# Performance work log

Hardware: AMD Instinct MI355X
Metric: run time of the kernel (lower is better)

## Reference

```python
import jax, jax.numpy as jnp
import numpy as np

EMB = 768

def setup_inputs() -> dict:
    key = jax.random.key(0)
    ks = jax.random.split(key, 9)
    B, N, E = 8, 2048, EMB
    s = 1.0 / np.sqrt(E)
    return {
        "x":  jax.random.normal(ks[0], (B, N, E), jnp.float32),
        "Wq": jax.random.normal(ks[1], (E, E), jnp.float32) * s,
        "bq": jnp.zeros((E,), jnp.float32),
        "Wk": jax.random.normal(ks[2], (E, E), jnp.float32) * s,
        "bk": jnp.zeros((E,), jnp.float32),
        "Wv": jax.random.normal(ks[3], (E, E), jnp.float32) * s,
        "bv": jnp.zeros((E,), jnp.float32),
        "Wo": jax.random.normal(ks[4], (E, E), jnp.float32) * s,
        "bo": jnp.zeros((E,), jnp.float32),
    }

def reference(x, Wq, bq, Wk, bk, Wv, bv, Wo, bo):
    # Single-head attention; scale uses full emb dim (as in the source).
    E = x.shape[-1]
    q = jnp.einsum('bne,ef->bnf', x, Wq) + bq
    k = jnp.einsum('bne,ef->bnf', x, Wk) + bk
    v = jnp.einsum('bne,ef->bnf', x, Wv) + bv
    scores = jnp.einsum('bqe,bke->bqk', q, k) / jnp.sqrt(jnp.asarray(E, x.dtype))
    attn = jax.nn.softmax(scores, axis=-1)  # dropout is identity in eval mode
    out = jnp.einsum('bqk,bke->bqe', attn, v)
    return jnp.einsum('bne,ef->bnf', out, Wo) + bo
```

## Files before the change

kernel.cpp:

```cpp
#include <hip/hip_runtime.h>
#include <hip/hip_fp16.h>
#include <stdint.h>

typedef unsigned short u16;
typedef __attribute__((ext_vector_type(8))) __bf16 bf16x8;
typedef __attribute__((ext_vector_type(4))) float f32x4;

#define SEQ 2048
#define EMB 768
#define NB  8
#define LDQK (2 * EMB)

__device__ __forceinline__ u16 f2bf(float f) {
  union { float f; uint32_t u; } a; a.f = f;
  uint32_t r = a.u + 0x7fffu + ((a.u >> 16) & 1u);
  return (u16)(r >> 16);
}
__device__ __forceinline__ float bf2f(u16 h) {
  union { uint32_t u; float f; } a; a.u = ((uint32_t)h) << 16;
  return a.f;
}

__global__ __launch_bounds__(256) void k_detect_bias(
    const u16* __restrict__ x, int* __restrict__ flag,
    const void* __restrict__ b0, const void* __restrict__ b1,
    const void* __restrict__ b2, const void* __restrict__ b3,
    float* __restrict__ biasf)
{
  const int tid = threadIdx.x;
  int bad = 0;
#pragma unroll
  for (int i = 0; i < 4; ++i) {
    const u16 h = x[(tid * 4 + i) * 2];
    const int e = (h >> 7) & 0xFF;
    bad += (e >= 160 && e <= 254) ? 1 : 0;
  }
#pragma unroll
  for (int off = 32; off > 0; off >>= 1) bad += __shfl_down(bad, off);
  __shared__ int cnt[4];
  __shared__ int sflag;
  if ((tid & 63) == 0) cnt[tid >> 6] = bad;
  __syncthreads();
  if (tid == 0) {
    const int f = (cnt[0] + cnt[1] + cnt[2] + cnt[3] > 200) ? 1 : 0;
    sflag = f;
    *flag = f;
  }
  __syncthreads();
  const int f32 = sflag;
#pragma unroll
  for (int z = 0; z < 4; ++z) {
    const void* src = (z == 0) ? b0 : (z == 1) ? b1 : (z == 2) ? b2 : b3;
#pragma unroll
    for (int i = 0; i < 3; ++i) {
      const int j = tid + i * 256;
      biasf[z * EMB + j] = f32 ? ((const float*)src)[j]
                               : bf2f(((const u16*)src)[j]);
    }
  }
}

__global__ __launch_bounds__(256) void k_convert_x(
    const void* __restrict__ src, u16* __restrict__ dst,
    const int* __restrict__ flag, int n4)
{
  const int i = blockIdx.x * 256 + threadIdx.x;
  if (i >= n4) return;
  if (*flag) {
    const float4 f = ((const float4*)src)[i];
    ushort4 o;
    o.x = f2bf(f.x); o.y = f2bf(f.y); o.z = f2bf(f.z); o.w = f2bf(f.w);
    ((ushort4*)dst)[i] = o;
  } else {
    ((ushort4*)dst)[i] = ((const ushort4*)src)[i];
  }
}

__global__ __launch_bounds__(256) void k_transpose_w(
    const void* __restrict__ W0, const void* __restrict__ W1,
    const void* __restrict__ W2, const void* __restrict__ W3,
    u16* __restrict__ WT, const int* __restrict__ flag)
{
  __shared__ u16 t[32][33];
  const int z = blockIdx.z;
  const void* in = (z == 0) ? W0 : (z == 1) ? W1 : (z == 2) ? W2 : W3;
  u16* out = WT + (size_t)z * EMB * EMB;
  const int c0 = blockIdx.x * 32, r0 = blockIdx.y * 32;
  const int tx = threadIdx.x, ty = threadIdx.y;
  const int f32 = *flag;
#pragma unroll
  for (int i = 0; i < 4; ++i) {
    const size_t idx = (size_t)(r0 + ty + i * 8) * EMB + c0 + tx;
    t[ty + i * 8][tx] = f32 ? f2bf(((const float*)in)[idx])
                            : ((const u16*)in)[idx];
  }
  __syncthreads();
#pragma unroll
  for (int i = 0; i < 4; ++i)
    out[(size_t)(c0 + ty + i * 8) * EMB + r0 + tx] = t[tx][ty + i * 8];
}

template <int EPI>
__device__ __forceinline__ void gemm_core(
    const u16* __restrict__ A, int lda,
    const u16* __restrict__ BT, int ldbt,
    void* __restrict__ Cp, int ldc,
    const float* __restrict__ biasf, const int* __restrict__ of32,
    float scale, int K, int m0, int n0)
{
  __shared__ __align__(16) u16 As[128 * 32];
  __shared__ __align__(16) u16 Bs[128 * 32];
  const int tid  = threadIdx.x;
  const int lane = tid & 63;
  const int wave = tid >> 6;
  const int wr   = (wave >> 1) * 64;
  const int wc   = (wave & 1) * 64;
  const int lrow = lane & 15;
  const int quad = lane >> 4;

  f32x4 acc[4][4];
#pragma unroll
  for (int i = 0; i < 4; ++i)
#pragma unroll
    for (int j = 0; j < 4; ++j)
#pragma unroll
      for (int r = 0; r < 4; ++r) acc[i][j][r] = 0.0f;

  for (int kt = 0; kt < K; kt += 32) {
#pragma unroll
    for (int i = 0; i < 2; ++i) {
      const int c = wave * 128 + i * 64 + lane;
      const int r = c >> 2, s = c & 3;
      const u16* ga = A  + (size_t)(m0 + r) * lda  + kt + s * 8;
      const u16* gb = BT + (size_t)(n0 + r) * ldbt + kt + s * 8;
      u16* la = As + (size_t)(wave * 128 + i * 64) * 8;
      u16* lb = Bs + (size_t)(wave * 128 + i * 64) * 8;
      __builtin_amdgcn_global_load_lds(
          (const __attribute__((address_space(1))) void*)ga,
          (__attribute__((address_space(3))) void*)la, 16, 0, 0);
      __builtin_amdgcn_global_load_lds(
          (const __attribute__((address_space(1))) void*)gb,
          (__attribute__((address_space(3))) void*)lb, 16, 0, 0);
    }
    __syncthreads();

    bf16x8 af[4], bfr[4];
#pragma unroll
    for (int i = 0; i < 4; ++i)
      af[i] = *(const bf16x8*)(As + (wr + i * 16 + lrow) * 32 + quad * 8);
#pragma unroll
    for (int j = 0; j < 4; ++j)
      bfr[j] = *(const bf16x8*)(Bs + (wc + j * 16 + lrow) * 32 + quad * 8);

#pragma unroll
    for (int i = 0; i < 4; ++i)
#pragma unroll
      for (int j = 0; j < 4; ++j)
        acc[i][j] = __builtin_amdgcn_mfma_f32_16x16x32_bf16(af[i], bfr[j],
                                                            acc[i][j], 0, 0, 0);
    __syncthreads();
  }

  if (EPI == 3) {
    u16* C = (u16*)Cp;
#pragma unroll
    for (int i = 0; i < 4; ++i)
#pragma unroll
      for (int j = 0; j < 4; ++j)
#pragma unroll
        for (int r = 0; r < 4; ++r) {
          const int row = m0 + wr + i * 16 + quad * 4 + r;
          const int col = n0 + wc + j * 16 + lrow;
          C[(size_t)row * ldc + col] =
              __half_as_ushort(__float2half(acc[i][j][r] * scale));
        }
  } else if (EPI == 2) {
    u16* C = (u16*)Cp;
#pragma unroll
    for (int i = 0; i < 4; ++i)
#pragma unroll
      for (int j = 0; j < 4; ++j)
#pragma unroll
        for (int r = 0; r < 4; ++r) {
          const int row = m0 + wr + i * 16 + quad * 4 + r;
          const int col = n0 + wc + j * 16 + lrow;
          C[(size_t)row * ldc + col] = f2bf(acc[i][j][r]);
        }
  } else if (EPI == 5) {
    u16* C = (u16*)Cp;
#pragma unroll
    for (int i = 0; i < 4; ++i)
#pragma unroll
      for (int r = 0; r < 4; ++r) {
        const int row = m0 + wr + i * 16 + quad * 4 + r;
        const float bv = biasf[row];
#pragma unroll
        for (int j = 0; j < 4; ++j) {
          const int col = n0 + wc + j * 16 + lrow;
          C[(size_t)row * ldc + col] = f2bf(acc[i][j][r] + bv);
        }
      }
  } else {
    float bv[4];
#pragma unroll
    for (int j = 0; j < 4; ++j) bv[j] = biasf[n0 + wc + j * 16 + lrow];
    const bool f32out = (of32 != nullptr) && (*of32 != 0);
    if (f32out) {
      float* C = (float*)Cp;
#pragma unroll
      for (int i = 0; i < 4; ++i)
#pragma unroll
        for (int j = 0; j < 4; ++j)
#pragma unroll
          for (int r = 0; r < 4; ++r) {
            const int row = m0 + wr + i * 16 + quad * 4 + r;
            const int col = n0 + wc + j * 16 + lrow;
            C[(size_t)row * ldc + col] = acc[i][j][r] + bv[j];
          }
    } else {
      u16* C = (u16*)Cp;
#pragma unroll
      for (int i = 0; i < 4; ++i)
#pragma unroll
        for (int j = 0; j < 4; ++j)
#pragma unroll
          for (int r = 0; r < 4; ++r) {
            const int row = m0 + wr + i * 16 + quad * 4 + r;
            const int col = n0 + wc + j * 16 + lrow;
            C[(size_t)row * ldc + col] = f2bf(acc[i][j][r] + bv[j]);
          }
    }
  }
}


__global__ __launch_bounds__(256) void k_gemm_qk(
    const u16* __restrict__ A, const u16* __restrict__ BT,
    u16* __restrict__ QK, const float* __restrict__ biasf)
{
  gemm_core<0>(A, EMB, BT, EMB, QK, LDQK, biasf, nullptr, 1.0f, EMB,
               blockIdx.y * 128, blockIdx.x * 128);
}

__global__ __launch_bounds__(256) void k_gemm_vt(
    const u16* __restrict__ WvT, const u16* __restrict__ xb,
    u16* __restrict__ VT, const float* __restrict__ biasv)
{
  const int b = blockIdx.z;
  gemm_core<5>(WvT, EMB,
               xb + (size_t)b * SEQ * EMB, EMB,
               VT + (size_t)b * EMB * SEQ, SEQ,
               biasv, nullptr, 1.0f, EMB,
               blockIdx.y * 128, blockIdx.x * 128);
}

__global__ __launch_bounds__(256) void k_gemm_out(
    const u16* __restrict__ A, const u16* __restrict__ BT,
    void* __restrict__ C, const float* __restrict__ biasf,
    const int* __restrict__ of32)
{
  gemm_core<0>(A, EMB, BT, EMB, C, EMB, biasf, of32, 1.0f, EMB,
               blockIdx.y * 128, blockIdx.x * 128);
}

__global__ __launch_bounds__(256) void k_gemm_scores(
    const u16* __restrict__ QK, u16* __restrict__ S, int b0)
{
  const int b = b0 + blockIdx.z;
  const u16* base = QK + (size_t)b * SEQ * LDQK;
  gemm_core<3>(base, LDQK,
               base + EMB, LDQK,
               S + (size_t)blockIdx.z * SEQ * SEQ, SEQ,
               nullptr, nullptr,
               0.03608439182435161f , EMB,
               blockIdx.y * 128, blockIdx.x * 128);
}

__global__ __launch_bounds__(256) void k_gemm_pv(
    const u16* __restrict__ P, const u16* __restrict__ VT,
    u16* __restrict__ O, int b0)
{
  const int b = b0 + blockIdx.z;
  gemm_core<2>(P  + (size_t)blockIdx.z * SEQ * SEQ, SEQ,
               VT + (size_t)b * EMB * SEQ, SEQ,
               O  + (size_t)b * SEQ * EMB, EMB,
               nullptr, nullptr, 1.0f, SEQ,
               blockIdx.y * 128, blockIdx.x * 128);
}

__global__ __launch_bounds__(256) void k_softmax(u16* __restrict__ S)
{
  u16* row = S + ((size_t)blockIdx.y * SEQ + blockIdx.x) * SEQ;
  const int tid = threadIdx.x;

  uint4 raw = *(const uint4*)(row + tid * 8);
  const u16* h = (const u16*)&raw;
  float v[8];
#pragma unroll
  for (int i = 0; i < 8; ++i) v[i] = __half2float(__ushort_as_half(h[i]));

  float mx = v[0];
#pragma unroll
  for (int i = 1; i < 8; ++i) mx = fmaxf(mx, v[i]);
#pragma unroll
  for (int off = 32; off > 0; off >>= 1) mx = fmaxf(mx, __shfl_down(mx, off));
  __shared__ float red[4], red2[4];
  if ((tid & 63) == 0) red[tid >> 6] = mx;
  __syncthreads();
  mx = fmaxf(fmaxf(red[0], red[1]), fmaxf(red[2], red[3]));

  float s = 0.0f;
#pragma unroll
  for (int i = 0; i < 8; ++i) { v[i] = __expf(v[i] - mx); s += v[i]; }
#pragma unroll
  for (int off = 32; off > 0; off >>= 1) s += __shfl_down(s, off);
  if ((tid & 63) == 0) red2[tid >> 6] = s;
  __syncthreads();
  s = red2[0] + red2[1] + red2[2] + red2[3];
  const float inv = 1.0f / s;

  uint4 outv;
  u16* o = (u16*)&outv;
#pragma unroll
  for (int i = 0; i < 8; ++i) o[i] = f2bf(v[i] * inv);
  *(uint4*)(row + tid * 8) = outv;
}


extern "C" void kernel_launch(void* const* d_in, const int* in_sizes, int n_in,
                              void* d_out, int out_size, void* d_ws, size_t ws_size,
                              hipStream_t stream)
{
  (void)in_sizes; (void)n_in; (void)out_size;
  const void* x  = d_in[0];
  const void* Wq = d_in[1];
  const void* bq = d_in[2];
  const void* Wk = d_in[3];
  const void* bk = d_in[4];
  const void* Wv = d_in[5];
  const void* bv = d_in[6];
  const void* Wo = d_in[7];
  const void* bo = d_in[8];

  char* ws = (char*)d_ws;
  size_t off = 0;
  auto alloc = [&](size_t bytes) -> void* {
    void* p = ws + off;
    off += (bytes + 255) & ~(size_t)255;
    return p;
  };
  int*   flag  = (int*)alloc(256);
  u16*   xb    = (u16*)alloc((size_t)NB * SEQ * EMB * 2);
  u16*   QK    = (u16*)alloc((size_t)NB * SEQ * LDQK * 2);
  u16*   VT    = (u16*)alloc((size_t)NB * EMB * SEQ * 2);
  u16*   O     = (u16*)alloc((size_t)NB * SEQ * EMB * 2);
  u16*   WT    = (u16*)alloc((size_t)4 * EMB * EMB * 2);
  float* biasf = (float*)alloc((size_t)4 * EMB * 4);
  u16*   S     = (u16*)(ws + off);
  size_t rem   = (ws_size > off) ? ws_size - off : 0;

  int GB = 8;
  while (GB > 1 && (size_t)GB * ((size_t)SEQ * SEQ * 2) > rem) GB >>= 1;

  k_detect_bias<<<1, 256, 0, stream>>>((const u16*)x, flag, bq, bk, bv, bo,
                                       biasf);
  const int n4 = NB * SEQ * EMB / 4;
  k_convert_x<<<(n4 + 255) / 256, 256, 0, stream>>>(x, xb, flag, n4);
  k_transpose_w<<<dim3(EMB / 32, EMB / 32, 4), dim3(32, 8), 0, stream>>>(
      Wq, Wk, Wv, Wo, WT, flag);

  k_gemm_qk<<<dim3(12, 128), 256, 0, stream>>>(xb, WT, QK, biasf);
  k_gemm_vt<<<dim3(16, 6, NB), 256, 0, stream>>>(
      WT + (size_t)2 * EMB * EMB, xb, VT, biasf + 2 * EMB);

  for (int g = 0; g < NB; g += GB) {
    k_gemm_scores<<<dim3(16, 16, GB), 256, 0, stream>>>(QK, S, g);
    k_softmax<<<dim3(SEQ, GB), 256, 0, stream>>>(S);
    k_gemm_pv<<<dim3(6, 16, GB), 256, 0, stream>>>(S, VT, O, g);
  }

  k_gemm_out<<<dim3(6, 128), 256, 0, stream>>>(O, WT + 3 * EMB * EMB, d_out,
                                               biasf + 3 * EMB, flag);
}
```

Baseline: 424.3 us.

## Double GEMM K-tile to 64 with XOR-swizzled LDS and XCD-aware block remap

The shared GEMM core now stages 64-wide K slices instead of 32, halving the number of barrier pairs per output tile. LDS reads use an XOR swizzle to avoid bank conflicts with the wider 128-byte rows. All GEMM kernels also remap their block IDs so consecutive logical tiles land on the same XCD, which should improve L2 reuse across the chiplets. The trade-off is doubled LDS use per block, which may lower occupancy. The remap assumes the total block count divides by 8.

```diff
diff --git a/kernel.cpp b/kernel.cpp
--- a/kernel.cpp
+++ b/kernel.cpp
@@ -19,6 +19,20 @@
 __device__ __forceinline__ float bf2f(u16 h) {
   union { uint32_t u; float f; } a; a.u = ((uint32_t)h) << 16;
   return a.f;
+}
+
+__device__ __forceinline__ void swz_bid(int& bx, int& by, int& bz)
+{
+  const int gx = gridDim.x, gy = gridDim.y;
+  const int nwg = gx * gy * gridDim.z;
+  const int lid = ((int)blockIdx.z * gy + (int)blockIdx.y) * gx +
+                  (int)blockIdx.x;
+  const int cpx = nwg >> 3;
+  const int orig = (lid & 7) * cpx + (lid >> 3);
+  bx = orig % gx;
+  const int t = orig / gx;
+  by = t % gy;
+  bz = t / gy;
 }
 
 __global__ __launch_bounds__(256) void k_detect_bias(
@@ -108,8 +122,8 @@
     const float* __restrict__ biasf, const int* __restrict__ of32,
     float scale, int K, int m0, int n0)
 {
-  __shared__ __align__(16) u16 As[128 * 32];
-  __shared__ __align__(16) u16 Bs[128 * 32];
+  __shared__ __align__(16) u16 As[128 * 64];
+  __shared__ __align__(16) u16 Bs[128 * 64];
   const int tid  = threadIdx.x;
   const int lane = tid & 63;
   const int wave = tid >> 6;
@@ -126,15 +140,16 @@
 #pragma unroll
       for (int r = 0; r < 4; ++r) acc[i][j][r] = 0.0f;
 
-  for (int kt = 0; kt < K; kt += 32) {
-#pragma unroll
-    for (int i = 0; i < 2; ++i) {
-      const int c = wave * 128 + i * 64 + lane;
-      const int r = c >> 2, s = c & 3;
-      const u16* ga = A  + (size_t)(m0 + r) * lda  + kt + s * 8;
-      const u16* gb = BT + (size_t)(n0 + r) * ldbt + kt + s * 8;
-      u16* la = As + (size_t)(wave * 128 + i * 64) * 8;
-      u16* lb = Bs + (size_t)(wave * 128 + i * 64) * 8;
+  for (int kt = 0; kt < K; kt += 64) {
+#pragma unroll
+    for (int i = 0; i < 4; ++i) {
+      const int c = wave * 256 + i * 64 + lane;
+      const int r = c >> 3, s = c & 7;
+      const int ss = s ^ (r & 7);
+      const u16* ga = A  + (size_t)(m0 + r) * lda  + kt + ss * 8;
+      const u16* gb = BT + (size_t)(n0 + r) * ldbt + kt + ss * 8;
+      u16* la = As + (size_t)(wave * 256 + i * 64) * 8;
+      u16* lb = Bs + (size_t)(wave * 256 + i * 64) * 8;
       __builtin_amdgcn_global_load_lds(
           (const __attribute__((address_space(1))) void*)ga,
           (__attribute__((address_space(3))) void*)la, 16, 0, 0);
@@ -144,20 +159,28 @@
     }
     __syncthreads();
 
-    bf16x8 af[4], bfr[4];
-#pragma unroll
-    for (int i = 0; i < 4; ++i)
-      af[i] = *(const bf16x8*)(As + (wr + i * 16 + lrow) * 32 + quad * 8);
-#pragma unroll
-    for (int j = 0; j < 4; ++j)
-      bfr[j] = *(const bf16x8*)(Bs + (wc + j * 16 + lrow) * 32 + quad * 8);
-
-#pragma unroll
-    for (int i = 0; i < 4; ++i)
-#pragma unroll
-      for (int j = 0; j < 4; ++j)
-        acc[i][j] = __builtin_amdgcn_mfma_f32_16x16x32_bf16(af[i], bfr[j],
-                                                            acc[i][j], 0, 0, 0);
+#pragma unroll
+    for (int kk = 0; kk < 2; ++kk) {
+      bf16x8 af[4], bfr[4];
+#pragma unroll
+      for (int i = 0; i < 4; ++i) {
+        const int row = wr + i * 16 + lrow;
+        const int cs  = ((kk << 2) + quad) ^ (lrow & 7);
+        af[i] = *(const bf16x8*)(As + row * 64 + cs * 8);
+      }
+#pragma unroll
+      for (int j = 0; j < 4; ++j) {
+        const int row = wc + j * 16 + lrow;
+        const int cs  = ((kk << 2) + quad) ^ (lrow & 7);
+        bfr[j] = *(const bf16x8*)(Bs + row * 64 + cs * 8);
+      }
+#pragma unroll
+      for (int i = 0; i < 4; ++i)
+#pragma unroll
+        for (int j = 0; j < 4; ++j)
+          acc[i][j] = __builtin_amdgcn_mfma_f32_16x16x32_bf16(
+              af[i], bfr[j], acc[i][j], 0, 0, 0);
+    }
     __syncthreads();
   }
 
@@ -238,20 +261,22 @@
     const u16* __restrict__ A, const u16* __restrict__ BT,
     u16* __restrict__ QK, const float* __restrict__ biasf)
 {
+  int bx, by, bz; swz_bid(bx, by, bz);
   gemm_core<0>(A, EMB, BT, EMB, QK, LDQK, biasf, nullptr, 1.0f, EMB,
-               blockIdx.y * 128, blockIdx.x * 128);
+               by * 128, bx * 128);
 }
 
 __global__ __launch_bounds__(256) void k_gemm_vt(
     const u16* __restrict__ WvT, const u16* __restrict__ xb,
     u16* __restrict__ VT, const float* __restrict__ biasv)
 {
-  const int b = blockIdx.z;
+  int bx, by, bz; swz_bid(bx, by, bz);
+  const int b = bz;
   gemm_core<5>(WvT, EMB,
                xb + (size_t)b * SEQ * EMB, EMB,
                VT + (size_t)b * EMB * SEQ, SEQ,
                biasv, nullptr, 1.0f, EMB,
-               blockIdx.y * 128, blockIdx.x * 128);
+               by * 128, bx * 128);
 }
 
 __global__ __launch_bounds__(256) void k_gemm_out(
@@ -259,33 +284,36 @@
     void* __restrict__ C, const float* __restrict__ biasf,
     const int* __restrict__ of32)
 {
+  int bx, by, bz; swz_bid(bx, by, bz);
   gemm_core<0>(A, EMB, BT, EMB, C, EMB, biasf, of32, 1.0f, EMB,
-               blockIdx.y * 128, blockIdx.x * 128);
+               by * 128, bx * 128);
 }
 
 __global__ __launch_bounds__(256) void k_gemm_scores(
     const u16* __restrict__ QK, u16* __restrict__ S, int b0)
 {
-  const int b = b0 + blockIdx.z;
+  int bx, by, bz; swz_bid(bx, by, bz);
+  const int b = b0 + bz;
   const u16* base = QK + (size_t)b * SEQ * LDQK;
   gemm_core<3>(base, LDQK,
                base + EMB, LDQK,
-               S + (size_t)blockIdx.z * SEQ * SEQ, SEQ,
+               S + (size_t)bz * SEQ * SEQ, SEQ,
                nullptr, nullptr,
                0.03608439182435161f , EMB,
-               blockIdx.y * 128, blockIdx.x * 128);
+               by * 128, bx * 128);
 }
 
 __global__ __launch_bounds__(256) void k_gemm_pv(
     const u16* __restrict__ P, const u16* __restrict__ VT,
     u16* __restrict__ O, int b0)
 {
-  const int b = b0 + blockIdx.z;
-  gemm_core<2>(P  + (size_t)blockIdx.z * SEQ * SEQ, SEQ,
+  int bx, by, bz; swz_bid(bx, by, bz);
+  const int b = b0 + bz;
+  gemm_core<2>(P  + (size_t)bz * SEQ * SEQ, SEQ,
                VT + (size_t)b * EMB * SEQ, SEQ,
                O  + (size_t)b * SEQ * EMB, EMB,
                nullptr, nullptr, 1.0f, SEQ,
-               blockIdx.y * 128, blockIdx.x * 128);
+               by * 128, bx * 128);
 }
 
 __global__ __launch_bounds__(256) void k_softmax(u16* __restrict__ S)
```

Result: faster. 402.4 us (-5.2%).
